# Optimization experiments

Hardware: AMD Instinct MI355X
Metric: run time of the kernel (lower is better)

## Reference

```python
import jax, jax.numpy as jnp
import numpy as np

N = 40000      # nodes
E = 640000     # edges
IN_DIM = 128
HID = 128
HEADS = 4
DHEAD = HID // HEADS  # 32
LAYERS = 3
TIMESTEPS = 2
NEG_SLOPE = 0.2


def setup_inputs() -> dict:
    key = jax.random.key(0)
    ks = jax.random.split(key, 16)
    s = 0.05
    inp = {
        "node_feats": jax.random.normal(ks[0], (N, IN_DIM), jnp.float32),
        "src": jax.random.randint(ks[1], (E,), 0, N, jnp.int32),
        "dst": jax.random.randint(ks[2], (E,), 0, N, jnp.int32),
        "proj_W": jax.random.normal(ks[3], (IN_DIM, HID), jnp.float32) * s,
        "proj_b": jnp.zeros((HID,), jnp.float32),
        "fc_W": jax.random.normal(ks[4], (LAYERS, HID, HID), jnp.float32) * s,
        "attn_l": jax.random.normal(ks[5], (LAYERS, HEADS, DHEAD), jnp.float32) * s,
        "attn_r": jax.random.normal(ks[6], (LAYERS, HEADS, DHEAD), jnp.float32) * s,
        "conv_bias": jnp.zeros((LAYERS, HID), jnp.float32),
        "gru_Wih": jax.random.normal(ks[7], (3 * HID, HID), jnp.float32) * s,
        "gru_Whh": jax.random.normal(ks[8], (3 * HID, HID), jnp.float32) * s,
        "gru_bih": jnp.zeros((3 * HID,), jnp.float32),
        "gru_bhh": jnp.zeros((3 * HID,), jnp.float32),
    }
    return inp


def _gat_layer(h, src, dst, fc_W, attn_l, attn_r, bias):
    # h: (N, HID). DGL GATConv: fc -> edge attn -> segment softmax -> scatter sum
    feat = (h @ fc_W).reshape(N, HEADS, DHEAD)
    el = jnp.einsum('nhd,hd->nh', feat, attn_l)  # (N, H)
    er = jnp.einsum('nhd,hd->nh', feat, attn_r)
    e = jax.nn.leaky_relu(el[src] + er[dst], NEG_SLOPE)  # (E, H)
    # segment softmax over incoming edges per destination node
    emax = jax.ops.segment_max(e, dst, num_segments=N)  # (N, H)
    ee = jnp.exp(e - emax[dst])
    denom = jax.ops.segment_sum(ee, dst, num_segments=N)
    alpha = ee / denom[dst]  # (E, H)
    msg = feat[src] * alpha[:, :, None]  # (E, H, D)
    rst = jax.ops.segment_sum(msg, dst, num_segments=N)  # (N, H, D)
    rst = rst + h.reshape(N, HEADS, DHEAD)          # identity residual
    rst = rst + bias.reshape(HEADS, DHEAD)          # learned bias
    return jax.nn.elu(rst).reshape(N, HID)


def _gru_step(x, Wih, Whh, bih, bhh):
    # seq_len == 1, h0 == 0 -> recurrent matmul Whh @ h0 vanishes; b_hh remains
    gi = x @ Wih.T + bih  # (N, 3*HID)
    r = jax.nn.sigmoid(gi[:, :HID] + bhh[:HID])
    z = jax.nn.sigmoid(gi[:, HID:2 * HID] + bhh[HID:2 * HID])
    n = jnp.tanh(gi[:, 2 * HID:] + r * bhh[2 * HID:])
    return (1.0 - z) * n


def reference(node_feats, src, dst, proj_W, proj_b, fc_W, attn_l, attn_r,
              conv_bias, gru_Wih, gru_Whh, gru_bih, gru_bhh):
    h = node_feats @ proj_W + proj_b
    for l in range(LAYERS):
        h = _gat_layer(h, src, dst, fc_W[l], attn_l[l], attn_r[l], conv_bias[l])
    for _ in range(TIMESTEPS):
        h = _gru_step(h, gru_Wih, gru_Whh, gru_bih, gru_bhh)
    return h
```

## Files before the change

kernel.cpp:

```cpp
#include <hip/hip_runtime.h>
#include <hip/hip_bf16.h>

#define NNODES 40000
#define NEDGES 640000
#define M2PAD  40064
#define HID    128
#define WSTRIDE (NEDGES + 16)

typedef __attribute__((ext_vector_type(8))) short bf16x8;
typedef __attribute__((ext_vector_type(4))) float f32x4;

__device__ __forceinline__ float bl(unsigned u){ return __uint_as_float(u << 16); }
__device__ __forceinline__ float bh(unsigned u){ return __uint_as_float(u & 0xFFFF0000u); }
__device__ __forceinline__ unsigned short f2b(float f){
    unsigned u = __float_as_uint(f);
    u = (u + 0x7FFFu + ((u >> 16) & 1u)) >> 16;
    return (unsigned short)u;
}
__device__ __forceinline__ float fast_rcp(float x){ return __builtin_amdgcn_rcpf(x); }

__device__ __forceinline__ void g2l16(const void* g, void* l){
    __builtin_amdgcn_global_load_lds(
        (const __attribute__((address_space(1))) unsigned int*)g,
        (__attribute__((address_space(3))) unsigned int*)l, 16, 0, 0);
}

__global__ void prep_all(const float* __restrict__ node_feats,
                         const float* __restrict__ proj_W, const float* __restrict__ fc_W,
                         const float* __restrict__ gru_Wih,
                         unsigned short* __restrict__ nf,
                         unsigned short* __restrict__ projWT, unsigned short* __restrict__ fcWT,
                         unsigned short* __restrict__ gruWb){
    int b = blockIdx.x;
    if (b < 5000){
        int gid = b * 256 + threadIdx.x;
        float4 v = ((const float4*)node_feats)[gid];
        ushort4 o;
        o.x = f2b(v.x); o.y = f2b(v.y); o.z = f2b(v.z); o.w = f2b(v.w);
        ((ushort4*)nf)[gid] = o;
    } else if (b < 5256){
        int t = b - 5000;
        int c = t >> 6;
        int idx = (t & 63) * 256 + threadIdx.x;
        const float* in   = (c == 0) ? proj_W : fc_W + (size_t)(c - 1) * 16384;
        unsigned short* o = (c == 0) ? projWT : fcWT + (size_t)(c - 1) * 16384;
        int k = idx >> 7, n = idx & 127;
        o[n * 128 + k] = f2b(in[idx]);
    } else {
        int idx = (b - 5256) * 256 + threadIdx.x;
        gruWb[idx] = f2b(gru_Wih[idx]);
    }
}

__global__ void count_kernel(const int* __restrict__ dst, int* __restrict__ deg){
    int e = blockIdx.x * 256 + threadIdx.x;
    atomicAdd(&deg[dst[e]], 1);
}

__global__ __launch_bounds__(1024) void scan_kernel(const int* __restrict__ deg,
        int* __restrict__ rowptr, int* __restrict__ cur, int Nn){
    __shared__ int wsum[17];
    __shared__ int carry;
    int t = threadIdx.x, lane = t & 63, wid = t >> 6;
    if (t == 0) carry = 0;
    __syncthreads();
    for (int base = 0; base < Nn; base += 1024){
        int idx = base + t;
        int v = (idx < Nn) ? deg[idx] : 0;
        int x = v;
        #pragma unroll
        for (int d = 1; d < 64; d <<= 1){
            int y = __shfl_up(x, d, 64);
            if (lane >= d) x += y;
        }
        if (lane == 63) wsum[wid] = x;
        __syncthreads();
        if (wid == 0){
            int vv = (lane < 16) ? wsum[lane] : 0;
            int xx = vv;
            #pragma unroll
            for (int d = 1; d < 16; d <<= 1){
                int y = __shfl_up(xx, d, 64);
                if (lane >= d) xx += y;
            }
            if (lane < 16) wsum[lane] = xx - vv;
            if (lane == 15) wsum[16] = xx;
        }
        __syncthreads();
        int excl = carry + wsum[wid] + (x - v);
        if (idx < Nn){ rowptr[idx] = excl; cur[idx] = excl; }
        __syncthreads();
        if (t == 0) carry += wsum[16];
        __syncthreads();
    }
    if (threadIdx.x == 0) rowptr[Nn] = carry;
}

__global__ void fill_kernel(const int* __restrict__ src, const int* __restrict__ dst,
                            int* __restrict__ cur, int* __restrict__ esrc,
                            int* __restrict__ edst){
    int e = blockIdx.x * 256 + threadIdx.x;
    int d = dst[e];
    int pos = atomicAdd(&cur[d], 1);
    esrc[pos] = src[e];
    edst[pos] = d;
}

template<int MT>
__global__ __launch_bounds__(256) void gemm_t(
        const unsigned short* __restrict__ A, const unsigned short* __restrict__ BT,
        const float* __restrict__ bias, void* __restrict__ C,
        int Mreal, int ldc, int outF32,
        const float* __restrict__ al, const float* __restrict__ ar,
        float* __restrict__ elp, float* __restrict__ erp)
{
    __shared__ unsigned char lds[MT * 256 + 32768];
    unsigned char* ldsA = lds;
    unsigned char* ldsB = lds + MT * 256;
    int w = threadIdx.x >> 6, lane = threadIdx.x & 63;
    int rsub = lane >> 4, c16 = lane & 15;
    long baseM = (long)blockIdx.x * MT;
    long baseN = (long)blockIdx.y * 128;

    #pragma unroll
    for (int i = 0; i < MT / 16; i++){
        int chunk = w * (MT / 16) + i;
        int r = chunk * 4 + rsub;
        int cg = c16 ^ (r & 15);
        long ar_ = baseM + r; if (ar_ >= Mreal) ar_ = Mreal - 1;
        g2l16((const unsigned char*)A + ar_ * 256 + cg * 16, ldsA + chunk * 1024);
    }
    #pragma unroll
    for (int i = 0; i < 8; i++){
        int chunk = w * 8 + i;
        int r = chunk * 4 + rsub;
        int cg = c16 ^ (r & 15);
        long br = baseN + r;
        g2l16((const unsigned char*)BT + br * 256 + cg * 16, ldsB + chunk * 1024);
    }
    __syncthreads();

    constexpr int MI = 4;
    constexpr int NI = (MT == 128) ? 4 : 2;
    int mo = (MT == 128) ? (w & 1) * 64 : 0;
    int no = (MT == 128) ? (w >> 1) * 64 : w * 32;
    int q = lane >> 4, cl = lane & 15;
    f32x4 acc[MI][NI];
    #pragma unroll
    for (int i = 0; i < MI; i++)
        #pragma unroll
        for (int j = 0; j < NI; j++) acc[i][j] = (f32x4){0.f, 0.f, 0.f, 0.f};

    #pragma unroll
    for (int kc = 0; kc < 4; kc++){
        bf16x8 av[MI], bv[NI];
        #pragma unroll
        for (int mi = 0; mi < MI; mi++){
            int row = mo + mi * 16 + cl;
            int cs = (kc * 4 + q) ^ (row & 15);
            av[mi] = *(const bf16x8*)(ldsA + row * 256 + cs * 16);
        }
        #pragma unroll
        for (int ni = 0; ni < NI; ni++){
            int row = no + ni * 16 + cl;
            int cs = (kc * 4 + q) ^ (row & 15);
            bv[ni] = *(const bf16x8*)(ldsB + row * 256 + cs * 16);
        }
        #pragma unroll
        for (int mi = 0; mi < MI; mi++)
            #pragma unroll
            for (int ni = 0; ni < NI; ni++)
                acc[mi][ni] = __builtin_amdgcn_mfma_f32_16x16x32_bf16(av[mi], bv[ni], acc[mi][ni], 0, 0, 0);
    }

    #pragma unroll
    for (int mi = 0; mi < MI; mi++){
        #pragma unroll
        for (int ni = 0; ni < NI; ni++){
            int gn = (int)baseN + no + ni * 16 + cl;
            float bvf = bias ? bias[gn] : 0.f;
            long gm0 = baseM + mo + mi * 16 + q * 4;
            #pragma unroll
            for (int reg = 0; reg < 4; reg++){
                float v = acc[mi][ni][reg] + bvf;
                long gm = gm0 + reg;
                if (gm < Mreal){
                    if (outF32) ((float*)C)[gm * ldc + gn] = v;
                    else ((unsigned short*)C)[gm * ldc + gn] = f2b(v);
                }
            }
        }
    }

    if (NI == 2 && al){
        float al_lo = al[no + cl], al_hi = al[no + 16 + cl];
        float ar_lo = ar[no + cl], ar_hi = ar[no + 16 + cl];
        #pragma unroll
        for (int mi = 0; mi < MI; mi++){
            #pragma unroll
            for (int reg = 0; reg < 4; reg++){
                float pl = acc[mi][0][reg] * al_lo + acc[mi][1][reg] * al_hi;
                float pr = acc[mi][0][reg] * ar_lo + acc[mi][1][reg] * ar_hi;
                #pragma unroll
                for (int msk = 8; msk; msk >>= 1){
                    pl += __shfl_xor(pl, msk, 64);
                    pr += __shfl_xor(pr, msk, 64);
                }
                long gm = baseM + mi * 16 + q * 4 + reg;
                if (cl == 0 && gm < Mreal){
                    elp[gm * 4 + w] = pl;
                    erp[gm * 4 + w] = pr;
                }
            }
        }
    }
}

__global__ __launch_bounds__(256) void gru_fused(
        const unsigned short* __restrict__ A, const unsigned short* __restrict__ BT,
        const float* __restrict__ bih, const float* __restrict__ bhh,
        void* __restrict__ out, int Mreal, int outF32)
{
    __shared__ unsigned char ldsA[16384];
    __shared__ unsigned char ldsB[32768];
    int w = threadIdx.x >> 6, lane = threadIdx.x & 63;
    int rsub = lane >> 4, c16 = lane & 15;
    long baseM = (long)blockIdx.x * 64;

    #pragma unroll
    for (int i = 0; i < 4; i++){
        int chunk = w * 4 + i;
        int r = chunk * 4 + rsub;
        int cg = c16 ^ (r & 15);
        long ar = baseM + r; if (ar >= Mreal) ar = Mreal - 1;
        g2l16((const unsigned char*)A + ar * 256 + cg * 16, ldsA + chunk * 1024);
    }

    int no = w * 32;
    int q = lane >> 4, cl = lane & 15;
    f32x4 acc[3][4][2];
    #pragma unroll
    for (int c = 0; c < 3; c++)
        #pragma unroll
        for (int i = 0; i < 4; i++)
            #pragma unroll
            for (int j = 0; j < 2; j++) acc[c][i][j] = (f32x4){0.f, 0.f, 0.f, 0.f};

    for (int c = 0; c < 3; c++){
        if (c) __syncthreads();
        #pragma unroll
        for (int i = 0; i < 8; i++){
            int chunk = w * 8 + i;
            int r = chunk * 4 + rsub;
            int cg = c16 ^ (r & 15);
            long br = c * 128 + r;
            g2l16((const unsigned char*)BT + br * 256 + cg * 16, ldsB + chunk * 1024);
        }
        __syncthreads();
        #pragma unroll
        for (int kc = 0; kc < 4; kc++){
            bf16x8 av[4], bv[2];
            #pragma unroll
            for (int mi = 0; mi < 4; mi++){
                int row = mi * 16 + cl;
                int cs = (kc * 4 + q) ^ (row & 15);
                av[mi] = *(const bf16x8*)(ldsA + row * 256 + cs * 16);
            }
            #pragma unroll
            for (int ni = 0; ni < 2; ni++){
                int row = no + ni * 16 + cl;
                int cs = (kc * 4 + q) ^ (row & 15);
                bv[ni] = *(const bf16x8*)(ldsB + row * 256 + cs * 16);
            }
            #pragma unroll
            for (int mi = 0; mi < 4; mi++)
                #pragma unroll
                for (int ni = 0; ni < 2; ni++)
                    acc[c][mi][ni] = __builtin_amdgcn_mfma_f32_16x16x32_bf16(av[mi], bv[ni], acc[c][mi][ni], 0, 0, 0);
        }
    }

    #pragma unroll
    for (int ni = 0; ni < 2; ni++){
        int j = no + ni * 16 + cl;
        float bir = bih[j]       + bhh[j];
        float biz = bih[128 + j] + bhh[128 + j];
        float bin = bih[256 + j];
        float bhn = bhh[256 + j];
        #pragma unroll
        for (int mi = 0; mi < 4; mi++){
            long gm0 = baseM + mi * 16 + q * 4;
            #pragma unroll
            for (int reg = 0; reg < 4; reg++){
                long n_row = gm0 + reg;
                float gr = acc[0][mi][ni][reg] + bir;
                float gz = acc[1][mi][ni][reg] + biz;
                float gn = acc[2][mi][ni][reg] + bin;
                float r = fast_rcp(1.f + __expf(-gr));
                float z = fast_rcp(1.f + __expf(-gz));
                float ex = __expf(2.f * (gn + r * bhn));
                float nn = (ex - 1.f) * fast_rcp(ex + 1.f);
                float v = (1.f - z) * nn;
                if (n_row < Mreal){
                    if (outF32) ((float*)out)[n_row * 128 + j] = v;
                    else ((unsigned short*)out)[n_row * 128 + j] = f2b(v);
                }
            }
        }
    }
}

__global__ void edge_w(const int* __restrict__ esrc, const int* __restrict__ edst,
                       const float* __restrict__ el, const float* __restrict__ er,
                       float* __restrict__ wgtT){
    int p = blockIdx.x * 256 + threadIdx.x;
    int sn = esrc[p], dn = edst[p];
    float4 l = *(const float4*)(el + (size_t)sn * 4);
    float4 r = *(const float4*)(er + (size_t)dn * 4);
    float e;
    e = l.x + r.x; e = (e > 0.f) ? e : 0.2f * e; wgtT[0 * WSTRIDE + p] = __expf(e);
    e = l.y + r.y; e = (e > 0.f) ? e : 0.2f * e; wgtT[1 * WSTRIDE + p] = __expf(e);
    e = l.z + r.z; e = (e > 0.f) ? e : 0.2f * e; wgtT[2 * WSTRIDE + p] = __expf(e);
    e = l.w + r.w; e = (e > 0.f) ? e : 0.2f * e; wgtT[3 * WSTRIDE + p] = __expf(e);
}

__global__ __launch_bounds__(256) void aggregate(
        const int* __restrict__ rowptr, const int* __restrict__ esrc,
        const float* __restrict__ wgtT,
        const unsigned short* __restrict__ feat, const float* __restrict__ bias,
        unsigned short* __restrict__ h)
{
    int wid = threadIdx.x >> 6, lane = threadIdx.x & 63;
    int n = blockIdx.x * 4 + wid;
    int hh = lane >> 4;
    int d0 = lane * 2;
    int beg = rowptr[n], end = rowptr[n + 1];
    float s = 0.f, a0 = 0.f, a1 = 0.f;
    const unsigned short* fb = feat + d0;
    const float* wplane = wgtT + (size_t)hh * WSTRIDE;

    if (beg < end){
        int p0 = beg & ~7;
        int4 sA = *(const int4*)(esrc + p0);
        int4 sB = *(const int4*)(esrc + p0 + 4);
        float4 wA = make_float4(0.f,0.f,0.f,0.f), wB = wA;
        unsigned f0=0,f1=0,f2=0,f3=0,f4=0,f5=0,f6=0,f7=0;
        int pg = p0 - 8;
        for (int p = p0; p < end; p += 8){
            float4 wcA = *(const float4*)(wplane + p);
            float4 wcB = *(const float4*)(wplane + p + 4);
            unsigned c0 = *(const unsigned*)(fb + (size_t)sA.x * 128);
            unsigned c1 = *(const unsigned*)(fb + (size_t)sA.y * 128);
            unsigned c2 = *(const unsigned*)(fb + (size_t)sA.z * 128);
            unsigned c3 = *(const unsigned*)(fb + (size_t)sA.w * 128);
            unsigned c4 = *(const unsigned*)(fb + (size_t)sB.x * 128);
            unsigned c5 = *(const unsigned*)(fb + (size_t)sB.y * 128);
            unsigned c6 = *(const unsigned*)(fb + (size_t)sB.z * 128);
            unsigned c7 = *(const unsigned*)(fb + (size_t)sB.w * 128);
            int4 nA = *(const int4*)(esrc + p + 8);
            int4 nB = *(const int4*)(esrc + p + 12);
            float w0 = (pg + 0 >= beg && pg + 0 < end) ? wA.x : 0.f;
            float w1 = (pg + 1 >= beg && pg + 1 < end) ? wA.y : 0.f;
            float w2 = (pg + 2 >= beg && pg + 2 < end) ? wA.z : 0.f;
            float w3 = (pg + 3 >= beg && pg + 3 < end) ? wA.w : 0.f;
            float w4 = (pg + 4 >= beg && pg + 4 < end) ? wB.x : 0.f;
            float w5 = (pg + 5 >= beg && pg + 5 < end) ? wB.y : 0.f;
            float w6 = (pg + 6 >= beg && pg + 6 < end) ? wB.z : 0.f;
            float w7 = (pg + 7 >= beg && pg + 7 < end) ? wB.w : 0.f;
            s += ((w0 + w1) + (w2 + w3)) + ((w4 + w5) + (w6 + w7));
            a0 = fmaf(w0, bl(f0), fmaf(w1, bl(f1), fmaf(w2, bl(f2), fmaf(w3, bl(f3), a0))));
            a0 = fmaf(w4, bl(f4), fmaf(w5, bl(f5), fmaf(w6, bl(f6), fmaf(w7, bl(f7), a0))));
            a1 = fmaf(w0, bh(f0), fmaf(w1, bh(f1), fmaf(w2, bh(f2), fmaf(w3, bh(f3), a1))));
            a1 = fmaf(w4, bh(f4), fmaf(w5, bh(f5), fmaf(w6, bh(f6), fmaf(w7, bh(f7), a1))));
            wA = wcA; wB = wcB;
            f0 = c0; f1 = c1; f2 = c2; f3 = c3; f4 = c4; f5 = c5; f6 = c6; f7 = c7;
            sA = nA; sB = nB; pg = p;
        }
        float w0 = (pg + 0 >= beg && pg + 0 < end) ? wA.x : 0.f;
        float w1 = (pg + 1 >= beg && pg + 1 < end) ? wA.y : 0.f;
        float w2 = (pg + 2 >= beg && pg + 2 < end) ? wA.z : 0.f;
        float w3 = (pg + 3 >= beg && pg + 3 < end) ? wA.w : 0.f;
        float w4 = (pg + 4 >= beg && pg + 4 < end) ? wB.x : 0.f;
        float w5 = (pg + 5 >= beg && pg + 5 < end) ? wB.y : 0.f;
        float w6 = (pg + 6 >= beg && pg + 6 < end) ? wB.z : 0.f;
        float w7 = (pg + 7 >= beg && pg + 7 < end) ? wB.w : 0.f;
        s += ((w0 + w1) + (w2 + w3)) + ((w4 + w5) + (w6 + w7));
        a0 = fmaf(w0, bl(f0), fmaf(w1, bl(f1), fmaf(w2, bl(f2), fmaf(w3, bl(f3), a0))));
        a0 = fmaf(w4, bl(f4), fmaf(w5, bl(f5), fmaf(w6, bl(f6), fmaf(w7, bl(f7), a0))));
        a1 = fmaf(w0, bh(f0), fmaf(w1, bh(f1), fmaf(w2, bh(f2), fmaf(w3, bh(f3), a1))));
        a1 = fmaf(w4, bh(f4), fmaf(w5, bh(f5), fmaf(w6, bh(f6), fmaf(w7, bh(f7), a1))));
    }
    float inv = (s > 0.f) ? fast_rcp(s) : 0.f;
    unsigned hv = *(const unsigned*)(h + (size_t)n * 128 + d0);
    float x0 = a0 * inv + bl(hv) + bias[d0];
    float x1 = a1 * inv + bh(hv) + bias[d0 + 1];
    x0 = (x0 > 0.f) ? x0 : expm1f(x0);
    x1 = (x1 > 0.f) ? x1 : expm1f(x1);
    unsigned outv = (unsigned)f2b(x0) | ((unsigned)f2b(x1) << 16);
    *(unsigned*)(h + (size_t)n * 128 + d0) = outv;
}

extern "C" void kernel_launch(void* const* d_in, const int* in_sizes, int n_in,
                              void* d_out, int out_size, void* d_ws, size_t ws_size,
                              hipStream_t stream) {
    const float* node_feats = (const float*)d_in[0];
    const int*   srcp       = (const int*)d_in[1];
    const int*   dstp       = (const int*)d_in[2];
    const float* proj_W     = (const float*)d_in[3];
    const float* proj_b     = (const float*)d_in[4];
    const float* fc_W       = (const float*)d_in[5];
    const float* attn_l     = (const float*)d_in[6];
    const float* attn_r     = (const float*)d_in[7];
    const float* conv_bias  = (const float*)d_in[8];
    const float* gru_Wih    = (const float*)d_in[9];
    const float* gru_bih    = (const float*)d_in[11];
    const float* gru_bhh    = (const float*)d_in[12];
    float* outp = (float*)d_out;

    char* ws = (char*)d_ws;
    size_t off = 0;
    auto carve = [&](size_t bytes) -> char* {
        char* p = ws + off;
        off += (bytes + 255) & ~(size_t)255;
        return p;
    };
    int*            deg    = (int*)carve((size_t)NNODES * 4);
    int*            rowptr = (int*)carve((size_t)(NNODES + 1) * 4);
    int*            cur    = (int*)carve((size_t)NNODES * 4);
    int*            esrc   = (int*)carve((size_t)(NEDGES + 16) * 4);
    int*            edst   = (int*)carve((size_t)NEDGES * 4);
    float*          el     = (float*)carve((size_t)NNODES * 4 * 4);
    float*          er     = (float*)carve((size_t)NNODES * 4 * 4);
    float*          wgtT   = (float*)carve((size_t)4 * WSTRIDE * 4);
    unsigned short* projWT = (unsigned short*)carve(16384 * 2);
    unsigned short* fcWT   = (unsigned short*)carve(3 * 16384 * 2);
    unsigned short* gruWb  = (unsigned short*)carve(49152 * 2);
    unsigned short* nf     = (unsigned short*)carve((size_t)NNODES * 128 * 2);
    unsigned short* h      = (unsigned short*)carve((size_t)M2PAD * 128 * 2);
    unsigned short* feat   = (unsigned short*)carve((size_t)M2PAD * 128 * 2);
    (void)ws_size; (void)in_sizes; (void)n_in; (void)out_size;

    hipMemsetAsync(deg, 0, (size_t)NNODES * 4, stream);
    prep_all<<<5448, 256, 0, stream>>>(node_feats, proj_W, fc_W, gru_Wih, nf, projWT, fcWT, gruWb);
    count_kernel<<<NEDGES / 256, 256, 0, stream>>>(dstp, deg);
    scan_kernel<<<1, 1024, 0, stream>>>(deg, rowptr, cur, NNODES);
    fill_kernel<<<NEDGES / 256, 256, 0, stream>>>(srcp, dstp, cur, esrc, edst);

    gemm_t<64><<<dim3(625, 1), 256, 0, stream>>>(nf, projWT, proj_b, h, NNODES, 128, 0,
                                                 nullptr, nullptr, nullptr, nullptr);

    for (int l = 0; l < 3; l++){
        gemm_t<64><<<dim3(625, 1), 256, 0, stream>>>(h, fcWT + l * 16384, nullptr, feat, NNODES, 128, 0,
                                                     attn_l + l * 128, attn_r + l * 128, el, er);
        edge_w<<<NEDGES / 256, 256, 0, stream>>>(esrc, edst, el, er, wgtT);
        aggregate<<<NNODES / 4, 256, 0, stream>>>(rowptr, esrc, wgtT, feat, conv_bias + l * 128, h);
    }

    gru_fused<<<625, 256, 0, stream>>>(h, gruWb, gru_bih, gru_bhh, h, NNODES, 0);
    gru_fused<<<625, 256, 0, stream>>>(h, gruWb, gru_bih, gru_bhh, outp, NNODES, 1);
}
```

Measured before the change: 403.8 us.

## Fuse degree count into prep, split aggregation across two waves, fuse GRU steps

Three changes in one. The degree-count atomics move into the prep kernel, which removes a launch. Aggregation now uses two waves per node, each taking alternating 8-edge chunks, and combines their partial sums through LDS; this doubles memory-level parallelism per node but adds a block barrier. The two GRU steps are fused into one kernel: the first step's output is written back into the swizzled LDS A tile in bf16, so the intermediate never goes to global memory, at the cost of reloading the B weights twice per block.

```diff
diff --git a/kernel.cpp b/kernel.cpp
--- a/kernel.cpp
+++ b/kernel.cpp
@@ -27,10 +27,10 @@
 
 __global__ void prep_all(const float* __restrict__ node_feats,
                          const float* __restrict__ proj_W, const float* __restrict__ fc_W,
-                         const float* __restrict__ gru_Wih,
+                         const float* __restrict__ gru_Wih, const int* __restrict__ dstp,
                          unsigned short* __restrict__ nf,
                          unsigned short* __restrict__ projWT, unsigned short* __restrict__ fcWT,
-                         unsigned short* __restrict__ gruWb){
+                         unsigned short* __restrict__ gruWb, int* __restrict__ deg){
     int b = blockIdx.x;
     if (b < 5000){
         int gid = b * 256 + threadIdx.x;
@@ -46,15 +46,13 @@
         unsigned short* o = (c == 0) ? projWT : fcWT + (size_t)(c - 1) * 16384;
         int k = idx >> 7, n = idx & 127;
         o[n * 128 + k] = f2b(in[idx]);
-    } else {
+    } else if (b < 5448){
         int idx = (b - 5256) * 256 + threadIdx.x;
         gruWb[idx] = f2b(gru_Wih[idx]);
-    }
-}
-
-__global__ void count_kernel(const int* __restrict__ dst, int* __restrict__ deg){
-    int e = blockIdx.x * 256 + threadIdx.x;
-    atomicAdd(&deg[dst[e]], 1);
+    } else {
+        int e = (b - 5448) * 256 + threadIdx.x;
+        atomicAdd(&deg[dstp[e]], 1);
+    }
 }
 
 __global__ __launch_bounds__(1024) void scan_kernel(const int* __restrict__ deg,
@@ -216,16 +214,18 @@
     }
 }
 
-__global__ __launch_bounds__(256) void gru_fused(
+__global__ __launch_bounds__(256) void gru2(
         const unsigned short* __restrict__ A, const unsigned short* __restrict__ BT,
         const float* __restrict__ bih, const float* __restrict__ bhh,
-        void* __restrict__ out, int Mreal, int outF32)
+        float* __restrict__ out, int Mreal)
 {
     __shared__ unsigned char ldsA[16384];
     __shared__ unsigned char ldsB[32768];
     int w = threadIdx.x >> 6, lane = threadIdx.x & 63;
     int rsub = lane >> 4, c16 = lane & 15;
     long baseM = (long)blockIdx.x * 64;
+    int no = w * 32;
+    int q = lane >> 4, cl = lane & 15;
 
     #pragma unroll
     for (int i = 0; i < 4; i++){
@@ -236,74 +236,79 @@
         g2l16((const unsigned char*)A + ar * 256 + cg * 16, ldsA + chunk * 1024);
     }
 
-    int no = w * 32;
-    int q = lane >> 4, cl = lane & 15;
-    f32x4 acc[3][4][2];
-    #pragma unroll
-    for (int c = 0; c < 3; c++)
-        #pragma unroll
-        for (int i = 0; i < 4; i++)
-            #pragma unroll
-            for (int j = 0; j < 2; j++) acc[c][i][j] = (f32x4){0.f, 0.f, 0.f, 0.f};
-
-    for (int c = 0; c < 3; c++){
-        if (c) __syncthreads();
-        #pragma unroll
-        for (int i = 0; i < 8; i++){
-            int chunk = w * 8 + i;
-            int r = chunk * 4 + rsub;
-            int cg = c16 ^ (r & 15);
-            long br = c * 128 + r;
-            g2l16((const unsigned char*)BT + br * 256 + cg * 16, ldsB + chunk * 1024);
-        }
-        __syncthreads();
-        #pragma unroll
-        for (int kc = 0; kc < 4; kc++){
-            bf16x8 av[4], bv[2];
+    for (int pass = 0; pass < 2; pass++){
+        f32x4 acc[3][4][2];
+        #pragma unroll
+        for (int c = 0; c < 3; c++)
+            #pragma unroll
+            for (int i = 0; i < 4; i++)
+                #pragma unroll
+                for (int j = 0; j < 2; j++) acc[c][i][j] = (f32x4){0.f, 0.f, 0.f, 0.f};
+
+        for (int c = 0; c < 3; c++){
+            __syncthreads();
+            #pragma unroll
+            for (int i = 0; i < 8; i++){
+                int chunk = w * 8 + i;
+                int r = chunk * 4 + rsub;
+                int cg = c16 ^ (r & 15);
+                long br = c * 128 + r;
+                g2l16((const unsigned char*)BT + br * 256 + cg * 16, ldsB + chunk * 1024);
+            }
+            __syncthreads();
+            #pragma unroll
+            for (int kc = 0; kc < 4; kc++){
+                bf16x8 av[4], bv[2];
+                #pragma unroll
+                for (int mi = 0; mi < 4; mi++){
+                    int row = mi * 16 + cl;
+                    int cs = (kc * 4 + q) ^ (row & 15);
+                    av[mi] = *(const bf16x8*)(ldsA + row * 256 + cs * 16);
+                }
+                #pragma unroll
+                for (int ni = 0; ni < 2; ni++){
+                    int row = no + ni * 16 + cl;
+                    int cs = (kc * 4 + q) ^ (row & 15);
+                    bv[ni] = *(const bf16x8*)(ldsB + row * 256 + cs * 16);
+                }
+                #pragma unroll
+                for (int mi = 0; mi < 4; mi++)
+                    #pragma unroll
+                    for (int ni = 0; ni < 2; ni++)
+                        acc[c][mi][ni] = __builtin_amdgcn_mfma_f32_16x16x32_bf16(av[mi], bv[ni], acc[c][mi][ni], 0, 0, 0);
+            }
+        }
+
+        if (pass == 0) __syncthreads();
+
+        #pragma unroll
+        for (int ni = 0; ni < 2; ni++){
+            int j = no + ni * 16 + cl;
+            float bir = bih[j]       + bhh[j];
+            float biz = bih[128 + j] + bhh[128 + j];
+            float bin = bih[256 + j];
+            float bhn = bhh[256 + j];
             #pragma unroll
             for (int mi = 0; mi < 4; mi++){
-                int row = mi * 16 + cl;
-                int cs = (kc * 4 + q) ^ (row & 15);
-                av[mi] = *(const bf16x8*)(ldsA + row * 256 + cs * 16);
-            }
-            #pragma unroll
-            for (int ni = 0; ni < 2; ni++){
-                int row = no + ni * 16 + cl;
-                int cs = (kc * 4 + q) ^ (row & 15);
-                bv[ni] = *(const bf16x8*)(ldsB + row * 256 + cs * 16);
-            }
-            #pragma unroll
-            for (int mi = 0; mi < 4; mi++)
-                #pragma unroll
-                for (int ni = 0; ni < 2; ni++)
-                    acc[c][mi][ni] = __builtin_amdgcn_mfma_f32_16x16x32_bf16(av[mi], bv[ni], acc[c][mi][ni], 0, 0, 0);
-        }
-    }
-
-    #pragma unroll
-    for (int ni = 0; ni < 2; ni++){
-        int j = no + ni * 16 + cl;
-        float bir = bih[j]       + bhh[j];
-        float biz = bih[128 + j] + bhh[128 + j];
-        float bin = bih[256 + j];
-        float bhn = bhh[256 + j];
-        #pragma unroll
-        for (int mi = 0; mi < 4; mi++){
-            long gm0 = baseM + mi * 16 + q * 4;
-            #pragma unroll
-            for (int reg = 0; reg < 4; reg++){
-                long n_row = gm0 + reg;
-                float gr = acc[0][mi][ni][reg] + bir;
-                float gz = acc[1][mi][ni][reg] + biz;
-                float gn = acc[2][mi][ni][reg] + bin;
-                float r = fast_rcp(1.f + __expf(-gr));
-                float z = fast_rcp(1.f + __expf(-gz));
-                float ex = __expf(2.f * (gn + r * bhn));
-                float nn = (ex - 1.f) * fast_rcp(ex + 1.f);
-                float v = (1.f - z) * nn;
-                if (n_row < Mreal){
-                    if (outF32) ((float*)out)[n_row * 128 + j] = v;
-                    else ((unsigned short*)out)[n_row * 128 + j] = f2b(v);
+                #pragma unroll
+                for (int reg = 0; reg < 4; reg++){
+                    int row = mi * 16 + q * 4 + reg;
+                    float gr = acc[0][mi][ni][reg] + bir;
+                    float gz = acc[1][mi][ni][reg] + biz;
+                    float gn = acc[2][mi][ni][reg] + bin;
+                    float r = fast_rcp(1.f + __expf(-gr));
+                    float z = fast_rcp(1.f + __expf(-gz));
+                    float ex = __expf(2.f * (gn + r * bhn));
+                    float nn = (ex - 1.f) * fast_rcp(ex + 1.f);
+                    float v = (1.f - z) * nn;
+                    if (pass == 0){
+                        int bc = j * 2;
+                        int addr = row * 256 + (((bc >> 4) ^ (row & 15)) << 4) + (bc & 15);
+                        *(unsigned short*)(ldsA + addr) = f2b(v);
+                    } else {
+                        long n_row = baseM + row;
+                        if (n_row < Mreal) out[n_row * 128 + j] = v;
+                    }
                 }
             }
         }
@@ -330,8 +335,10 @@
         const unsigned short* __restrict__ feat, const float* __restrict__ bias,
         unsigned short* __restrict__ h)
 {
-    int wid = threadIdx.x >> 6, lane = threadIdx.x & 63;
-    int n = blockIdx.x * 4 + wid;
+    __shared__ float red[2][3][64];
+    int wv = threadIdx.x >> 6, lane = threadIdx.x & 63;
+    int nsub = wv >> 1, half = wv & 1;
+    int n = blockIdx.x * 2 + nsub;
     int hh = lane >> 4;
     int d0 = lane * 2;
     int beg = rowptr[n], end = rowptr[n + 1];
@@ -339,14 +346,14 @@
     const unsigned short* fb = feat + d0;
     const float* wplane = wgtT + (size_t)hh * WSTRIDE;
 
-    if (beg < end){
-        int p0 = beg & ~7;
+    int p0 = (beg & ~7) + half * 8;
+    if (p0 < end){
         int4 sA = *(const int4*)(esrc + p0);
         int4 sB = *(const int4*)(esrc + p0 + 4);
         float4 wA = make_float4(0.f,0.f,0.f,0.f), wB = wA;
         unsigned f0=0,f1=0,f2=0,f3=0,f4=0,f5=0,f6=0,f7=0;
-        int pg = p0 - 8;
-        for (int p = p0; p < end; p += 8){
+        int pg = p0 - 16;
+        for (int p = p0; p < end; p += 16){
             float4 wcA = *(const float4*)(wplane + p);
             float4 wcB = *(const float4*)(wplane + p + 4);
             unsigned c0 = *(const unsigned*)(fb + (size_t)sA.x * 128);
@@ -357,8 +364,8 @@
             unsigned c5 = *(const unsigned*)(fb + (size_t)sB.y * 128);
             unsigned c6 = *(const unsigned*)(fb + (size_t)sB.z * 128);
             unsigned c7 = *(const unsigned*)(fb + (size_t)sB.w * 128);
-            int4 nA = *(const int4*)(esrc + p + 8);
-            int4 nB = *(const int4*)(esrc + p + 12);
+            int4 nA = *(const int4*)(esrc + p + 16);
+            int4 nB = *(const int4*)(esrc + p + 20);
             float w0 = (pg + 0 >= beg && pg + 0 < end) ? wA.x : 0.f;
             float w1 = (pg + 1 >= beg && pg + 1 < end) ? wA.y : 0.f;
             float w2 = (pg + 2 >= beg && pg + 2 < end) ? wA.z : 0.f;
@@ -390,14 +397,26 @@
         a1 = fmaf(w0, bh(f0), fmaf(w1, bh(f1), fmaf(w2, bh(f2), fmaf(w3, bh(f3), a1))));
         a1 = fmaf(w4, bh(f4), fmaf(w5, bh(f5), fmaf(w6, bh(f6), fmaf(w7, bh(f7), a1))));
     }
-    float inv = (s > 0.f) ? fast_rcp(s) : 0.f;
-    unsigned hv = *(const unsigned*)(h + (size_t)n * 128 + d0);
-    float x0 = a0 * inv + bl(hv) + bias[d0];
-    float x1 = a1 * inv + bh(hv) + bias[d0 + 1];
-    x0 = (x0 > 0.f) ? x0 : expm1f(x0);
-    x1 = (x1 > 0.f) ? x1 : expm1f(x1);
-    unsigned outv = (unsigned)f2b(x0) | ((unsigned)f2b(x1) << 16);
-    *(unsigned*)(h + (size_t)n * 128 + d0) = outv;
+
+    if (half){
+        red[nsub][0][lane] = s;
+        red[nsub][1][lane] = a0;
+        red[nsub][2][lane] = a1;
+    }
+    __syncthreads();
+    if (!half){
+        s  += red[nsub][0][lane];
+        a0 += red[nsub][1][lane];
+        a1 += red[nsub][2][lane];
+        float inv = (s > 0.f) ? fast_rcp(s) : 0.f;
+        unsigned hv = *(const unsigned*)(h + (size_t)n * 128 + d0);
+        float x0 = a0 * inv + bl(hv) + bias[d0];
+        float x1 = a1 * inv + bh(hv) + bias[d0 + 1];
+        x0 = (x0 > 0.f) ? x0 : expm1f(x0);
+        x1 = (x1 > 0.f) ? x1 : expm1f(x1);
+        unsigned outv = (unsigned)f2b(x0) | ((unsigned)f2b(x1) << 16);
+        *(unsigned*)(h + (size_t)n * 128 + d0) = outv;
+    }
 }
 
 extern "C" void kernel_launch(void* const* d_in, const int* in_sizes, int n_in,
@@ -427,7 +446,7 @@
     int*            deg    = (int*)carve((size_t)NNODES * 4);
     int*            rowptr = (int*)carve((size_t)(NNODES + 1) * 4);
     int*            cur    = (int*)carve((size_t)NNODES * 4);
-    int*            esrc   = (int*)carve((size_t)(NEDGES + 16) * 4);
+    int*            esrc   = (int*)carve((size_t)(NEDGES + 32) * 4);
     int*            edst   = (int*)carve((size_t)NEDGES * 4);
     float*          el     = (float*)carve((size_t)NNODES * 4 * 4);
     float*          er     = (float*)carve((size_t)NNODES * 4 * 4);
@@ -441,8 +460,9 @@
     (void)ws_size; (void)in_sizes; (void)n_in; (void)out_size;
 
     hipMemsetAsync(deg, 0, (size_t)NNODES * 4, stream);
-    prep_all<<<5448, 256, 0, stream>>>(node_feats, proj_W, fc_W, gru_Wih, nf, projWT, fcWT, gruWb);
-    count_kernel<<<NEDGES / 256, 256, 0, stream>>>(dstp, deg);
+    hipMemsetAsync(esrc + NEDGES, 0, 32 * 4, stream);
+    prep_all<<<7948, 256, 0, stream>>>(node_feats, proj_W, fc_W, gru_Wih, dstp,
+                                       nf, projWT, fcWT, gruWb, deg);
     scan_kernel<<<1, 1024, 0, stream>>>(deg, rowptr, cur, NNODES);
     fill_kernel<<<NEDGES / 256, 256, 0, stream>>>(srcp, dstp, cur, esrc, edst);
 
@@ -453,9 +473,8 @@
         gemm_t<64><<<dim3(625, 1), 256, 0, stream>>>(h, fcWT + l * 16384, nullptr, feat, NNODES, 128, 0,
                                                      attn_l + l * 128, attn_r + l * 128, el, er);
         edge_w<<<NEDGES / 256, 256, 0, stream>>>(esrc, edst, el, er, wgtT);
-        aggregate<<<NNODES / 4, 256, 0, stream>>>(rowptr, esrc, wgtT, feat, conv_bias + l * 128, h);
-    }
-
-    gru_fused<<<625, 256, 0, stream>>>(h, gruWb, gru_bih, gru_bhh, h, NNODES, 0);
-    gru_fused<<<625, 256, 0, stream>>>(h, gruWb, gru_bih, gru_bhh, outp, NNODES, 1);
-}
+        aggregate<<<NNODES / 2, 256, 0, stream>>>(rowptr, esrc, wgtT, feat, conv_bias + l * 128, h);
+    }
+
+    gru2<<<625, 256, 0, stream>>>(h, gruWb, gru_bih, gru_bhh, outp, NNODES);
+}
```

Measured after the change: 439.8 us. 8.9% more time.
